# Kernel optimization log

Measured on AMD Instinct MI355X. Metric: run time of the kernel, lower is better.

Reference implementation:

```python
import jax, jax.numpy as jnp
import numpy as np

B, S, E = 4, 2048, 1024
H = 16
D = E // H  # head_dim = 64


def setup_inputs() -> dict:
    key = jax.random.key(0)
    k1, k2, k3 = jax.random.split(key, 3)
    x = jax.random.normal(k1, (B, S, E), dtype=jnp.float32)
    w_qkv = jax.random.normal(k2, (E, 3 * E), dtype=jnp.float32) * (E ** -0.5)
    b_qkv = jnp.zeros((3 * E,), dtype=jnp.float32)
    w_proj = jax.random.normal(k3, (E, E), dtype=jnp.float32) * (E ** -0.5)
    b_proj = jnp.zeros((E,), dtype=jnp.float32)
    return {"x": x, "w_qkv": w_qkv, "b_qkv": b_qkv, "w_proj": w_proj, "b_proj": b_proj}


def reference(x, w_qkv, b_qkv, w_proj, b_proj):
    bsz, seq_len, emb = x.shape
    scale = D ** -0.5
    qkv = x @ w_qkv + b_qkv                      # [B,S,3E]
    q, k, v = jnp.split(qkv, 3, axis=2)
    # [B,S,E] -> [B,H,S,D]
    q = q.reshape(bsz, seq_len, H, D).transpose(0, 2, 1, 3)
    k = k.reshape(bsz, seq_len, H, D).transpose(0, 2, 1, 3)
    v = v.reshape(bsz, seq_len, H, D).transpose(0, 2, 1, 3)
    att = jnp.einsum('bhqd,bhkd->bhqk', q, k) * scale
    causal = jnp.tril(jnp.ones((seq_len, seq_len), dtype=bool))
    att = jnp.where(causal, att, -jnp.inf)
    att = jax.nn.softmax(att, axis=-1)
    y = jnp.einsum('bhqk,bhkd->bhqd', att, v)
    y = y.transpose(0, 2, 1, 3).reshape(bsz, seq_len, emb)
    return y @ w_proj + b_proj
```

## Files before the change

### kernel.cpp

```cpp
#include <hip/hip_runtime.h>
#include <hip/hip_bf16.h>
#include <stdint.h>

#define S_LEN 2048
#define EMB   1024
#define NH    16
#define HD    64

typedef unsigned short u16;
typedef __attribute__((ext_vector_type(4))) float f32x4;
typedef __attribute__((ext_vector_type(8))) short bf16x8;

typedef __attribute__((address_space(1))) const unsigned char gas_t;
typedef __attribute__((address_space(3))) unsigned char las_t;

static __device__ __forceinline__ void gld_lds16(const void* g, void* l) {
  __builtin_amdgcn_global_load_lds((gas_t*)g, (las_t*)l, 16, 0, 0);
}

static __device__ __forceinline__ u16 f2bf(float f) {
  unsigned int u = __builtin_bit_cast(unsigned int, f);
  u = u + 0x7fffu + ((u >> 16) & 1u);
  return (u16)(u >> 16);
}

static __device__ __forceinline__ float fexp2(float x) {
  float r;
  asm("v_exp_f32 %0, %1" : "=v"(r) : "v"(x));
  return r;
}

static __device__ __forceinline__ unsigned cvt_pk_bf16(float lo, float hi) {
  unsigned r;
  asm("v_cvt_pk_bf16_f32 %0, %1, %2" : "=v"(r) : "v"(lo), "v"(hi));
  return r;
}

template <int CTRL>
static __device__ __forceinline__ float dppmax(float x) {
  int s = __builtin_amdgcn_update_dpp(0, __builtin_bit_cast(int, x), CTRL, 0xf, 0xf, true);
  return fmaxf(x, __builtin_bit_cast(float, s));
}
template <int CTRL>
static __device__ __forceinline__ float dppadd(float x) {
  int s = __builtin_amdgcn_update_dpp(0, __builtin_bit_cast(int, x), CTRL, 0xf, 0xf, true);
  return x + __builtin_bit_cast(float, s);
}
static __device__ __forceinline__ float red16_max(float x) {
  x = dppmax<0xB1>(x); x = dppmax<0x4E>(x);
  x = dppmax<0x140>(x); x = dppmax<0x141>(x);
  return x;
}
static __device__ __forceinline__ float red16_sum(float x) {
  x = dppadd<0xB1>(x); x = dppadd<0x4E>(x);
  x = dppadd<0x140>(x); x = dppadd<0x141>(x);
  return x;
}

__global__ __launch_bounds__(256) void k_cvt(const float* __restrict__ in,
                                             u16* __restrict__ out, int n4) {
  int i = blockIdx.x * blockDim.x + threadIdx.x;
  int stride = gridDim.x * blockDim.x;
  for (; i < n4; i += stride) {
    float4 f = ((const float4*)in)[i];
    ushort4 o;
    o.x = f2bf(f.x); o.y = f2bf(f.y); o.z = f2bf(f.z); o.w = f2bf(f.w);
    ((ushort4*)out)[i] = o;
  }
}

__global__ __launch_bounds__(256) void k_transpose_cvt(const float* __restrict__ W,
                                                       u16* __restrict__ WT,
                                                       int K, int N) {
  __shared__ u16 tile[64][68];
  const int c0 = blockIdx.x * 64, r0 = blockIdx.y * 64;
  const int t = threadIdx.x;
  const int tr = t >> 4, tc4 = (t & 15) * 4;
#pragma unroll
  for (int i = 0; i < 4; i++) {
    const int r = tr + 16 * i;
    float4 f = *(const float4*)&W[(size_t)(r0 + r) * N + c0 + tc4];
    ushort4 o;
    o.x = f2bf(f.x); o.y = f2bf(f.y); o.z = f2bf(f.z); o.w = f2bf(f.w);
    *(ushort4*)&tile[r][tc4] = o;
  }
  __syncthreads();
  const int oc = t >> 2, or0 = (t & 3) * 16;
  u16 vals[16];
#pragma unroll
  for (int j = 0; j < 16; j++) vals[j] = tile[or0 + j][oc];
  u16* dst = &WT[(size_t)(c0 + oc) * K + r0 + or0];
  *(uint4*)dst = *(const uint4*)&vals[0];
  *(uint4*)(dst + 8) = *(const uint4*)&vals[8];
}

template <int MODE>
__global__ __launch_bounds__(256) void k_gemm(const u16* __restrict__ A,
                                              const u16* __restrict__ BT,
                                              const float* __restrict__ bias,
                                              float* __restrict__ Cout,
                                              u16* __restrict__ q_ws,
                                              u16* __restrict__ k_ws,
                                              u16* __restrict__ v_t,
                                              int N, int K) {
  __shared__ u16 As[2][128 * 32];
  __shared__ u16 Bs[2][128 * 32];
  const int tid = threadIdx.x;
  const int w = tid >> 6, lane = tid & 63;
  const int wr = w >> 1, wc = w & 1;
  const int lrow = lane & 15, lk8 = (lane >> 4) * 8;
  const int brow = blockIdx.y * 128, bcol = blockIdx.x * 128;
  const int srow = lane >> 2;
  const int scol = (lane & 3) * 8;

  const f32x4 zero = {0.f, 0.f, 0.f, 0.f};
  f32x4 acc[4][4];
#pragma unroll
  for (int m = 0; m < 4; m++)
#pragma unroll
    for (int n = 0; n < 4; n++) acc[m][n] = zero;

  auto stage = [&](int kt, int buf) {
#pragma unroll
    for (int i = 0; i < 2; i++) {
      const int c = w * 2 + i;
      const int row = c * 16 + srow;
      gld_lds16(&A[(size_t)(brow + row) * K + kt + scol], (void*)(&As[buf][c * 512]));
      gld_lds16(&BT[(size_t)(bcol + row) * K + kt + scol], (void*)(&Bs[buf][c * 512]));
    }
  };

  const int NK = K >> 5;
  stage(0, 0);
  __syncthreads();
  for (int it = 0; it < NK; ++it) {
    const int cur = it & 1;
    if (it + 1 < NK) stage((it + 1) << 5, cur ^ 1);
    bf16x8 af[4], bfr[4];
#pragma unroll
    for (int mt = 0; mt < 4; mt++)
      af[mt] = *(const bf16x8*)&As[cur][(wr * 64 + mt * 16 + lrow) * 32 + lk8];
#pragma unroll
    for (int nt = 0; nt < 4; nt++)
      bfr[nt] = *(const bf16x8*)&Bs[cur][(wc * 64 + nt * 16 + lrow) * 32 + lk8];
    __builtin_amdgcn_s_setprio(1);
#pragma unroll
    for (int mt = 0; mt < 4; mt++)
#pragma unroll
      for (int nt = 0; nt < 4; nt++)
        acc[mt][nt] = __builtin_amdgcn_mfma_f32_16x16x32_bf16(af[mt], bfr[nt],
                                                              acc[mt][nt], 0, 0, 0);
    __builtin_amdgcn_s_setprio(0);
    __syncthreads();
  }

  if constexpr (MODE == 0) {
    const int which = bcol >> 10;
#pragma unroll
    for (int mt = 0; mt < 4; mt++)
#pragma unroll
      for (int nt = 0; nt < 4; nt++) {
        const int col = bcol + wc * 64 + nt * 16 + lrow;
        const int e = col & 1023;
        const int h = e >> 6, d = e & 63;
        const int row0 = brow + wr * 64 + mt * 16 + (lane >> 4) * 4;
        const int b = row0 >> 11, s0 = row0 & 2047;
        const size_t bh = (size_t)(b * NH + h);
        const float bv = bias[col];
        if (which == 2) {
          ushort4 pk;
          pk.x = f2bf(acc[mt][nt][0] + bv);
          pk.y = f2bf(acc[mt][nt][1] + bv);
          pk.z = f2bf(acc[mt][nt][2] + bv);
          pk.w = f2bf(acc[mt][nt][3] + bv);
          *(ushort4*)&v_t[(bh * HD + d) * S_LEN + s0] = pk;
        } else {
          u16* dst = which ? k_ws : q_ws;
#pragma unroll
          for (int r = 0; r < 4; r++)
            dst[(bh * S_LEN + s0 + r) * HD + d] = f2bf(acc[mt][nt][r] + bv);
        }
      }
  } else {
#pragma unroll
    for (int mt = 0; mt < 4; mt++)
#pragma unroll
      for (int nt = 0; nt < 4; nt++)
#pragma unroll
        for (int r = 0; r < 4; r++) {
          const int row = brow + wr * 64 + mt * 16 + (lane >> 4) * 4 + r;
          const int col = bcol + wc * 64 + nt * 16 + lrow;
          Cout[(size_t)row * N + col] = acc[mt][nt][r] + bias[col];
        }
  }
}

__global__ __launch_bounds__(256, 2) void k_attn(const u16* __restrict__ q_ws,
                                                 const u16* __restrict__ k_ws,
                                                 const u16* __restrict__ v_t,
                                                 u16* __restrict__ y) {
  __shared__ u16 Kl[2][64 * 64];
  __shared__ u16 Vl[2][64 * 64];
  __shared__ u16 Pl[4][16 * 64];
  const int tid = threadIdx.x;
  const int w = tid >> 6, lane = tid & 63;
  const int lrow = lane & 15, lk8 = (lane >> 4) * 8;
  const int qrow_t = (lane >> 4) * 4;
  const int pr = blockIdx.x;
  const int tileA = pr, tileB = 31 - pr;
  const int bh = blockIdx.y;
  const size_t base = (size_t)bh * S_LEN * HD;
  const float SC = 0.125f * 1.4426950408889634f;

  bf16x8 qfA[2], qfB[2];
#pragma unroll
  for (int ks = 0; ks < 2; ks++) {
    qfA[ks] = *(const bf16x8*)&q_ws[base + (size_t)(tileA * 64 + w * 16 + lrow) * HD + ks * 32 + lk8];
    qfB[ks] = *(const bf16x8*)&q_ws[base + (size_t)(tileB * 64 + w * 16 + lrow) * HD + ks * 32 + lk8];
  }

  const f32x4 zero = {0.f, 0.f, 0.f, 0.f};
  f32x4 oA[4], oB[4];
#pragma unroll
  for (int dt = 0; dt < 4; dt++) { oA[dt] = zero; oB[dt] = zero; }
  float mA[4], lA[4], mB[4], lB[4];
#pragma unroll
  for (int r = 0; r < 4; r++) { mA[r] = -1e30f; lA[r] = 0.f; mB[r] = -1e30f; lB[r] = 0.f; }

  u16* Pw = &Pl[w][0];

  auto stage = [&](int jb, int buf) {
#pragma unroll
    for (int i = 0; i < 2; i++) {
      const int c = w * 2 + i;
      const int row = c * 8 + (lane >> 3);
      const int blk = (lane & 7) ^ (row & 7);
      gld_lds16(&k_ws[base + (size_t)(jb * 64 + row) * HD + blk * 8],
                (void*)(&Kl[buf][c * 512]));
      gld_lds16(&v_t[base + (size_t)row * S_LEN + jb * 64 + blk * 8],
                (void*)(&Vl[buf][c * 512]));
    }
  };

  auto process = [&](int cur, const bf16x8 (&kf)[2][4], const bf16x8 (&qf)[2],
                     f32x4 (&o)[4], float (&m_run)[4], float (&l_run)[4],
                     bool maskDiag) {
    f32x4 sa[4];
#pragma unroll
    for (int nt = 0; nt < 4; nt++) sa[nt] = zero;
    __builtin_amdgcn_s_setprio(1);
#pragma unroll
    for (int ks = 0; ks < 2; ks++)
#pragma unroll
      for (int nt = 0; nt < 4; nt++)
        sa[nt] = __builtin_amdgcn_mfma_f32_16x16x32_bf16(qf[ks], kf[ks][nt], sa[nt], 0, 0, 0);
    __builtin_amdgcn_s_setprio(0);

    float sv[4][4];
#pragma unroll
    for (int nt = 0; nt < 4; nt++)
#pragma unroll
      for (int r = 0; r < 4; r++) {
        float x = sa[nt][r] * SC;
        if (maskDiag && (nt * 16 + lrow) > (w * 16 + qrow_t + r)) x = -3.0e38f;
        sv[nt][r] = x;
      }

#pragma unroll
    for (int r = 0; r < 4; r++) {
      float mx = fmaxf(fmaxf(sv[0][r], sv[1][r]), fmaxf(sv[2][r], sv[3][r]));
      mx = red16_max(mx);
      const float mn = fmaxf(m_run[r], mx);
      const float alpha = fexp2(m_run[r] - mn);
      float sum = 0.f;
#pragma unroll
      for (int nt = 0; nt < 4; nt++) {
        const float p = fexp2(sv[nt][r] - mn);
        sv[nt][r] = p;
        sum += p;
      }
      sum = red16_sum(sum);
      l_run[r] = l_run[r] * alpha + sum;
      m_run[r] = mn;
#pragma unroll
      for (int dt = 0; dt < 4; dt++) o[dt][r] *= alpha;
    }

#pragma unroll
    for (int nt = 0; nt < 4; nt++) {
      const unsigned pk0 = cvt_pk_bf16(sv[nt][0], sv[nt][1]);
      const unsigned pk1 = cvt_pk_bf16(sv[nt][2], sv[nt][3]);
      const int col2 = (nt * 16 + lrow) * 2;
      char* pb = (char*)Pw;
      *(u16*)(pb + (qrow_t + 0) * 128 + (col2 ^ (((qrow_t + 0) & 7) << 4))) = (u16)pk0;
      *(u16*)(pb + (qrow_t + 1) * 128 + (col2 ^ (((qrow_t + 1) & 7) << 4))) = (u16)(pk0 >> 16);
      *(u16*)(pb + (qrow_t + 2) * 128 + (col2 ^ (((qrow_t + 2) & 7) << 4))) = (u16)pk1;
      *(u16*)(pb + (qrow_t + 3) * 128 + (col2 ^ (((qrow_t + 3) & 7) << 4))) = (u16)(pk1 >> 16);
    }

    __builtin_amdgcn_s_setprio(1);
#pragma unroll
    for (int ks = 0; ks < 2; ks++) {
      const int blk = (ks * 4 + (lane >> 4)) ^ (lrow & 7);
      bf16x8 pf = *(const bf16x8*)((const char*)Pw + lrow * 128 + blk * 16);
#pragma unroll
      for (int dt = 0; dt < 4; dt++) {
        const int vr = dt * 16 + lrow;
        const int vblk = (ks * 4 + (lane >> 4)) ^ (vr & 7);
        bf16x8 vf = *(const bf16x8*)&Vl[cur][vr * 64 + vblk * 8];
        o[dt] = __builtin_amdgcn_mfma_f32_16x16x32_bf16(pf, vf, o[dt], 0, 0, 0);
      }
    }
    __builtin_amdgcn_s_setprio(0);
  };

  stage(0, 0);
  __syncthreads();
  for (int jb = 0; jb <= tileB; jb++) {
    const int cur = jb & 1;
    if (jb < tileB) stage(jb + 1, cur ^ 1);
    bf16x8 kf[2][4];
#pragma unroll
    for (int ks = 0; ks < 2; ks++)
#pragma unroll
      for (int nt = 0; nt < 4; nt++) {
        const int kvr = nt * 16 + lrow;
        const int blk = (ks * 4 + (lane >> 4)) ^ (kvr & 7);
        kf[ks][nt] = *(const bf16x8*)&Kl[cur][kvr * 64 + blk * 8];
      }
    process(cur, kf, qfB, oB, mB, lB, jb == tileB);
    if (jb <= tileA) process(cur, kf, qfA, oA, mA, lA, jb == tileA);
    __syncthreads();
  }

  const int b = bh >> 4, h = bh & 15;
#pragma unroll
  for (int r = 0; r < 4; r++) {
    const float invA = 1.0f / lA[r];
    const float invB = 1.0f / lB[r];
    const int qgA = tileA * 64 + w * 16 + qrow_t + r;
    const int qgB = tileB * 64 + w * 16 + qrow_t + r;
#pragma unroll
    for (int dt = 0; dt < 4; dt++) {
      y[((size_t)(b * S_LEN + qgA)) * EMB + h * HD + dt * 16 + lrow] = f2bf(oA[dt][r] * invA);
      y[((size_t)(b * S_LEN + qgB)) * EMB + h * HD + dt * 16 + lrow] = f2bf(oB[dt][r] * invB);
    }
  }
}

extern "C" void kernel_launch(void* const* d_in, const int* in_sizes, int n_in,
                              void* d_out, int out_size, void* d_ws, size_t ws_size,
                              hipStream_t stream) {
  const float* x      = (const float*)d_in[0];
  const float* w_qkv  = (const float*)d_in[1];
  const float* b_qkv  = (const float*)d_in[2];
  const float* w_proj = (const float*)d_in[3];
  const float* b_proj = (const float*)d_in[4];
  float* out = (float*)d_out;

  char* ws = (char*)d_ws;
  u16* wqkvT  = (u16*)(ws);
  u16* wprojT = (u16*)(ws + 6291456);
  u16* xb     = (u16*)(ws + 8388608);
  u16* q_ws   = (u16*)(ws + 25165824);
  u16* k_ws   = (u16*)(ws + 41943040);
  u16* v_t    = (u16*)(ws + 58720256);
  u16* y_att  = xb;

  k_cvt<<<dim3(1024), dim3(256), 0, stream>>>(x, xb, (8192 * 1024) / 4);
  k_transpose_cvt<<<dim3(48, 16), dim3(256), 0, stream>>>(w_qkv, wqkvT, 1024, 3072);
  k_transpose_cvt<<<dim3(16, 16), dim3(256), 0, stream>>>(w_proj, wprojT, 1024, 1024);
  k_gemm<0><<<dim3(24, 64), dim3(256), 0, stream>>>(xb, wqkvT, b_qkv, nullptr,
                                                    q_ws, k_ws, v_t, 3072, 1024);
  k_attn<<<dim3(16, 64), dim3(256), 0, stream>>>(q_ws, k_ws, v_t, y_att);
  k_gemm<1><<<dim3(8, 64), dim3(256), 0, stream>>>(y_att, wprojT, b_proj, out,
                                                   nullptr, nullptr, nullptr, 1024, 1024);
}
```

Measured before the change: 216.1 us.

## Compute transposed scores so softmax P stays in registers via permlane swaps

Swaps the MFMA operand order so each lane holds one query row's scores across key columns. The row max and sum then reduce with permlane32/16 swaps over four lane groups instead of per-row DPP reductions. The P tile is repacked into the PV operand layout with permlane swaps rather than written to and read back from LDS, removing the Pl shared buffer and its stores and loads. Output stores become 8-byte vector writes. The risk is in getting the register shuffle mapping right, plus the cost of the extra permlane instructions.

```diff
diff --git a/kernel.cpp b/kernel.cpp
--- a/kernel.cpp
+++ b/kernel.cpp
@@ -36,25 +36,25 @@
   return r;
 }
 
-template <int CTRL>
-static __device__ __forceinline__ float dppmax(float x) {
-  int s = __builtin_amdgcn_update_dpp(0, __builtin_bit_cast(int, x), CTRL, 0xf, 0xf, true);
-  return fmaxf(x, __builtin_bit_cast(float, s));
-}
-template <int CTRL>
-static __device__ __forceinline__ float dppadd(float x) {
-  int s = __builtin_amdgcn_update_dpp(0, __builtin_bit_cast(int, x), CTRL, 0xf, 0xf, true);
-  return x + __builtin_bit_cast(float, s);
-}
-static __device__ __forceinline__ float red16_max(float x) {
-  x = dppmax<0xB1>(x); x = dppmax<0x4E>(x);
-  x = dppmax<0x140>(x); x = dppmax<0x141>(x);
-  return x;
-}
-static __device__ __forceinline__ float red16_sum(float x) {
-  x = dppadd<0xB1>(x); x = dppadd<0x4E>(x);
-  x = dppadd<0x140>(x); x = dppadd<0x141>(x);
-  return x;
+static __device__ __forceinline__ float red4rows_max(float x) {
+  unsigned u = __builtin_bit_cast(unsigned, x);
+  auto r = __builtin_amdgcn_permlane32_swap(u, u, false, false);
+  float y = fmaxf(__builtin_bit_cast(float, (unsigned)r[0]),
+                  __builtin_bit_cast(float, (unsigned)r[1]));
+  unsigned v = __builtin_bit_cast(unsigned, y);
+  auto r2 = __builtin_amdgcn_permlane16_swap(v, v, false, false);
+  return fmaxf(__builtin_bit_cast(float, (unsigned)r2[0]),
+               __builtin_bit_cast(float, (unsigned)r2[1]));
+}
+static __device__ __forceinline__ float red4rows_sum(float x) {
+  unsigned u = __builtin_bit_cast(unsigned, x);
+  auto r = __builtin_amdgcn_permlane32_swap(u, u, false, false);
+  float y = __builtin_bit_cast(float, (unsigned)r[0]) +
+            __builtin_bit_cast(float, (unsigned)r[1]);
+  unsigned v = __builtin_bit_cast(unsigned, y);
+  auto r2 = __builtin_amdgcn_permlane16_swap(v, v, false, false);
+  return __builtin_bit_cast(float, (unsigned)r2[0]) +
+         __builtin_bit_cast(float, (unsigned)r2[1]);
 }
 
 __global__ __launch_bounds__(256) void k_cvt(const float* __restrict__ in,
@@ -201,11 +201,10 @@
                                                  u16* __restrict__ y) {
   __shared__ u16 Kl[2][64 * 64];
   __shared__ u16 Vl[2][64 * 64];
-  __shared__ u16 Pl[4][16 * 64];
   const int tid = threadIdx.x;
   const int w = tid >> 6, lane = tid & 63;
   const int lrow = lane & 15, lk8 = (lane >> 4) * 8;
-  const int qrow_t = (lane >> 4) * 4;
+  const int g4 = (lane >> 4) * 4;
   const int pr = blockIdx.x;
   const int tileA = pr, tileB = 31 - pr;
   const int bh = blockIdx.y;
@@ -223,11 +222,7 @@
   f32x4 oA[4], oB[4];
 #pragma unroll
   for (int dt = 0; dt < 4; dt++) { oA[dt] = zero; oB[dt] = zero; }
-  float mA[4], lA[4], mB[4], lB[4];
-#pragma unroll
-  for (int r = 0; r < 4; r++) { mA[r] = -1e30f; lA[r] = 0.f; mB[r] = -1e30f; lB[r] = 0.f; }
-
-  u16* Pw = &Pl[w][0];
+  float mA = -1e30f, lA = 0.f, mB = -1e30f, lB = 0.f;
 
   auto stage = [&](int jb, int buf) {
 #pragma unroll
@@ -243,8 +238,7 @@
   };
 
   auto process = [&](int cur, const bf16x8 (&kf)[2][4], const bf16x8 (&qf)[2],
-                     f32x4 (&o)[4], float (&m_run)[4], float (&l_run)[4],
-                     bool maskDiag) {
+                     f32x4 (&o)[4], float& m_run, float& l_run, bool maskDiag) {
     f32x4 sa[4];
 #pragma unroll
     for (int nt = 0; nt < 4; nt++) sa[nt] = zero;
@@ -253,7 +247,7 @@
     for (int ks = 0; ks < 2; ks++)
 #pragma unroll
       for (int nt = 0; nt < 4; nt++)
-        sa[nt] = __builtin_amdgcn_mfma_f32_16x16x32_bf16(qf[ks], kf[ks][nt], sa[nt], 0, 0, 0);
+        sa[nt] = __builtin_amdgcn_mfma_f32_16x16x32_bf16(kf[ks][nt], qf[ks], sa[nt], 0, 0, 0);
     __builtin_amdgcn_s_setprio(0);
 
     float sv[4][4];
@@ -262,55 +256,64 @@
 #pragma unroll
       for (int r = 0; r < 4; r++) {
         float x = sa[nt][r] * SC;
-        if (maskDiag && (nt * 16 + lrow) > (w * 16 + qrow_t + r)) x = -3.0e38f;
+        if (maskDiag && (nt * 16 + g4 + r) > (w * 16 + lrow)) x = -3.0e38f;
         sv[nt][r] = x;
       }
 
-#pragma unroll
-    for (int r = 0; r < 4; r++) {
-      float mx = fmaxf(fmaxf(sv[0][r], sv[1][r]), fmaxf(sv[2][r], sv[3][r]));
-      mx = red16_max(mx);
-      const float mn = fmaxf(m_run[r], mx);
-      const float alpha = fexp2(m_run[r] - mn);
-      float sum = 0.f;
-#pragma unroll
-      for (int nt = 0; nt < 4; nt++) {
+    float mx = fmaxf(fmaxf(fmaxf(sv[0][0], sv[0][1]), fmaxf(sv[0][2], sv[0][3])),
+                     fmaxf(fmaxf(sv[1][0], sv[1][1]), fmaxf(sv[1][2], sv[1][3])));
+    mx = fmaxf(mx,
+               fmaxf(fmaxf(fmaxf(sv[2][0], sv[2][1]), fmaxf(sv[2][2], sv[2][3])),
+                     fmaxf(fmaxf(sv[3][0], sv[3][1]), fmaxf(sv[3][2], sv[3][3]))));
+    mx = red4rows_max(mx);
+    const float mn = fmaxf(m_run, mx);
+    const float alpha = fexp2(m_run - mn);
+    float sum = 0.f;
+#pragma unroll
+    for (int nt = 0; nt < 4; nt++)
+#pragma unroll
+      for (int r = 0; r < 4; r++) {
         const float p = fexp2(sv[nt][r] - mn);
         sv[nt][r] = p;
         sum += p;
       }
-      sum = red16_sum(sum);
-      l_run[r] = l_run[r] * alpha + sum;
-      m_run[r] = mn;
-#pragma unroll
-      for (int dt = 0; dt < 4; dt++) o[dt][r] *= alpha;
+    sum = red4rows_sum(sum);
+    l_run = l_run * alpha + sum;
+    m_run = mn;
+#pragma unroll
+    for (int dt = 0; dt < 4; dt++) o[dt] *= alpha;
+
+    unsigned pk[4][2];
+#pragma unroll
+    for (int nt = 0; nt < 4; nt++) {
+      pk[nt][0] = cvt_pk_bf16(sv[nt][0], sv[nt][1]);
+      pk[nt][1] = cvt_pk_bf16(sv[nt][2], sv[nt][3]);
     }
-
-#pragma unroll
-    for (int nt = 0; nt < 4; nt++) {
-      const unsigned pk0 = cvt_pk_bf16(sv[nt][0], sv[nt][1]);
-      const unsigned pk1 = cvt_pk_bf16(sv[nt][2], sv[nt][3]);
-      const int col2 = (nt * 16 + lrow) * 2;
-      char* pb = (char*)Pw;
-      *(u16*)(pb + (qrow_t + 0) * 128 + (col2 ^ (((qrow_t + 0) & 7) << 4))) = (u16)pk0;
-      *(u16*)(pb + (qrow_t + 1) * 128 + (col2 ^ (((qrow_t + 1) & 7) << 4))) = (u16)(pk0 >> 16);
-      *(u16*)(pb + (qrow_t + 2) * 128 + (col2 ^ (((qrow_t + 2) & 7) << 4))) = (u16)pk1;
-      *(u16*)(pb + (qrow_t + 3) * 128 + (col2 ^ (((qrow_t + 3) & 7) << 4))) = (u16)(pk1 >> 16);
+    union { unsigned u[4]; bf16x8 v; } c0, c1;
+    {
+      auto r0 = __builtin_amdgcn_permlane32_swap(pk[0][0], pk[1][0], false, false);
+      auto s0 = __builtin_amdgcn_permlane16_swap(r0[0], r0[1], false, false);
+      auto r1 = __builtin_amdgcn_permlane32_swap(pk[0][1], pk[1][1], false, false);
+      auto s1 = __builtin_amdgcn_permlane16_swap(r1[0], r1[1], false, false);
+      c0.u[0] = s0[0]; c0.u[1] = s1[0]; c0.u[2] = s0[1]; c0.u[3] = s1[1];
+      auto r2 = __builtin_amdgcn_permlane32_swap(pk[2][0], pk[3][0], false, false);
+      auto s2 = __builtin_amdgcn_permlane16_swap(r2[0], r2[1], false, false);
+      auto r3 = __builtin_amdgcn_permlane32_swap(pk[2][1], pk[3][1], false, false);
+      auto s3 = __builtin_amdgcn_permlane16_swap(r3[0], r3[1], false, false);
+      c1.u[0] = s2[0]; c1.u[1] = s3[0]; c1.u[2] = s2[1]; c1.u[3] = s3[1];
     }
+    bf16x8 pfrag[2] = {c0.v, c1.v};
 
     __builtin_amdgcn_s_setprio(1);
 #pragma unroll
-    for (int ks = 0; ks < 2; ks++) {
-      const int blk = (ks * 4 + (lane >> 4)) ^ (lrow & 7);
-      bf16x8 pf = *(const bf16x8*)((const char*)Pw + lrow * 128 + blk * 16);
+    for (int ks = 0; ks < 2; ks++)
 #pragma unroll
       for (int dt = 0; dt < 4; dt++) {
         const int vr = dt * 16 + lrow;
         const int vblk = (ks * 4 + (lane >> 4)) ^ (vr & 7);
         bf16x8 vf = *(const bf16x8*)&Vl[cur][vr * 64 + vblk * 8];
-        o[dt] = __builtin_amdgcn_mfma_f32_16x16x32_bf16(pf, vf, o[dt], 0, 0, 0);
-      }
-    }
+        o[dt] = __builtin_amdgcn_mfma_f32_16x16x32_bf16(vf, pfrag[ks], o[dt], 0, 0, 0);
+      }
     __builtin_amdgcn_s_setprio(0);
   };
 
@@ -334,17 +337,19 @@
   }
 
   const int b = bh >> 4, h = bh & 15;
-#pragma unroll
-  for (int r = 0; r < 4; r++) {
-    const float invA = 1.0f / lA[r];
-    const float invB = 1.0f / lB[r];
-    const int qgA = tileA * 64 + w * 16 + qrow_t + r;
-    const int qgB = tileB * 64 + w * 16 + qrow_t + r;
-#pragma unroll
-    for (int dt = 0; dt < 4; dt++) {
-      y[((size_t)(b * S_LEN + qgA)) * EMB + h * HD + dt * 16 + lrow] = f2bf(oA[dt][r] * invA);
-      y[((size_t)(b * S_LEN + qgB)) * EMB + h * HD + dt * 16 + lrow] = f2bf(oB[dt][r] * invB);
-    }
+  const float invA = 1.0f / lA;
+  const float invB = 1.0f / lB;
+  const int qgA = tileA * 64 + w * 16 + lrow;
+  const int qgB = tileB * 64 + w * 16 + lrow;
+#pragma unroll
+  for (int dt = 0; dt < 4; dt++) {
+    ushort4 sA, sB;
+    sA.x = f2bf(oA[dt][0] * invA); sA.y = f2bf(oA[dt][1] * invA);
+    sA.z = f2bf(oA[dt][2] * invA); sA.w = f2bf(oA[dt][3] * invA);
+    sB.x = f2bf(oB[dt][0] * invB); sB.y = f2bf(oB[dt][1] * invB);
+    sB.z = f2bf(oB[dt][2] * invB); sB.w = f2bf(oB[dt][3] * invB);
+    *(ushort4*)&y[(size_t)(b * S_LEN + qgA) * EMB + h * HD + dt * 16 + g4] = sA;
+    *(ushort4*)&y[(size_t)(b * S_LEN + qgB) * EMB + h * HD + dt * 16 + g4] = sB;
   }
 }
 
```

New measurement: 201.9 us. -6.6%, faster.
